# Optimization experiments

Hardware: AMD Instinct MI355X
Metric: run time of the kernel (lower is better)

## Reference

```python
import jax, jax.numpy as jnp
import numpy as np

HID, HEADS, LAYERS, EDIM = 128, 2, 3, 1
HEAD_DIM = HID  # out_channels per head (concat=False -> mean over heads)
N_NODES, N_EDGES = 50000, 500000
LN_EPS = 1e-5


def _layer_norm(x, g, b):
    mu = x.mean(-1, keepdims=True)
    var = ((x - mu) ** 2).mean(-1, keepdims=True)
    return (x - mu) * jax.lax.rsqrt(var + LN_EPS) * g + b


def _transformer_conv(x, src, tgt, edge_attr, Wq, bq, Wk, bk, Wv, bv, We, Wskip, bskip):
    # PyG TransformerConv, concat=False, root_weight=True, lin_edge bias=False
    N = x.shape[0]
    E = src.shape[0]
    q = (x @ Wq + bq).reshape(N, HEADS, HEAD_DIM)
    k = (x @ Wk + bk).reshape(N, HEADS, HEAD_DIM)
    v = (x @ Wv + bv).reshape(N, HEADS, HEAD_DIM)
    e = (edge_attr @ We).reshape(E, HEADS, HEAD_DIM)          # [E,H,C]
    k_j = k[src] + e                                          # gather + edge bias
    q_i = q[tgt]
    alpha = (q_i * k_j).sum(-1) / jnp.sqrt(jnp.asarray(HEAD_DIM, x.dtype))  # [E,H]
    # scatter-softmax over incoming edges of each target node
    m = jax.ops.segment_max(alpha, tgt, num_segments=N)       # [N,H]
    a = jnp.exp(alpha - m[tgt])
    denom = jax.ops.segment_sum(a, tgt, num_segments=N)
    a = a / jnp.where(denom[tgt] > 0, denom[tgt], 1.0)
    msg = (v[src] + e) * a[..., None]                         # [E,H,C]
    out = jax.ops.segment_sum(msg, tgt, num_segments=N)       # [N,H,C]
    out = out.mean(axis=1)                                    # concat=False -> head mean
    return out + x @ Wskip + bskip                            # root/skip connection


def reference(x, edge_index, edge_attr, ln_in_g, ln_in_b,
              Wq, bq, Wk, bk, Wv, bv, We, Wskip, bskip, ln_g, ln_b):
    src, tgt = edge_index[0], edge_index[1]
    x = _layer_norm(x, ln_in_g, ln_in_b)
    for l in range(LAYERS):
        h = _transformer_conv(x, src, tgt, edge_attr,
                              Wq[l], bq[l], Wk[l], bk[l], Wv[l], bv[l],
                              We[l], Wskip[l], bskip[l])
        h = jax.nn.elu(h)
        x = _layer_norm(x + h, ln_g[l], ln_b[l])
    return x


def setup_inputs() -> dict:
    key = jax.random.key(0)
    ks = jax.random.split(key, 12)
    HC = HEADS * HEAD_DIM
    s = 1.0 / np.sqrt(HID)
    inp = {
        "x": jax.random.normal(ks[0], (N_NODES, HID), jnp.float32),
        "edge_index": jax.random.randint(ks[1], (2, N_EDGES), 0, N_NODES, jnp.int64),
        "edge_attr": jax.random.normal(ks[2], (N_EDGES, EDIM), jnp.float32),
        "ln_in_g": jnp.ones((HID,), jnp.float32),
        "ln_in_b": jnp.zeros((HID,), jnp.float32),
        "Wq": jax.random.normal(ks[3], (LAYERS, HID, HC), jnp.float32) * s,
        "bq": jnp.zeros((LAYERS, HC), jnp.float32),
        "Wk": jax.random.normal(ks[4], (LAYERS, HID, HC), jnp.float32) * s,
        "bk": jnp.zeros((LAYERS, HC), jnp.float32),
        "Wv": jax.random.normal(ks[5], (LAYERS, HID, HC), jnp.float32) * s,
        "bv": jnp.zeros((LAYERS, HC), jnp.float32),
        "We": jax.random.normal(ks[6], (LAYERS, EDIM, HC), jnp.float32),
        "Wskip": jax.random.normal(ks[7], (LAYERS, HID, HID), jnp.float32) * s,
        "bskip": jnp.zeros((LAYERS, HID), jnp.float32),
        "ln_g": jnp.ones((LAYERS, HID), jnp.float32),
        "ln_b": jnp.zeros((LAYERS, HID), jnp.float32),
    }
    return inp
```

## Files before the change

kernel.cpp:

```cpp
#include <hip/hip_runtime.h>
#include <math.h>

#define NN 50000
#define NE 500000
#define HIDS 128
#define MCOLS 896
#define NLAYERS 3

typedef __attribute__((ext_vector_type(8))) short short8;
typedef __attribute__((ext_vector_type(4))) float floatx4;
typedef _Float16 half8v __attribute__((ext_vector_type(8)));

#define BSTR 152

static __device__ __forceinline__ unsigned short f2bf(float f) {
    unsigned u = __float_as_uint(f);
    u += 0x7fffu + ((u >> 16) & 1u);
    return (unsigned short)(u >> 16);
}
static __device__ __forceinline__ unsigned short f2h(float f) {
    union { _Float16 h; unsigned short u; } c;
    c.h = (_Float16)f;
    return c.u;
}
#define DPP_ADD(v, ctrl) \
    v += __int_as_float(__builtin_amdgcn_mov_dpp(__float_as_int(v), ctrl, 0xf, 0xf, true))
static __device__ __forceinline__ float wred16(float v) {
    DPP_ADD(v, 0xB1);
    DPP_ADD(v, 0x4E);
    DPP_ADD(v, 0x124);
    DPP_ADD(v, 0x128);
    return v;
}
static __device__ __forceinline__ float wred64(float v) {
    v += __shfl_xor(v, 1, 64);
    v += __shfl_xor(v, 2, 64);
    v += __shfl_xor(v, 4, 64);
    v += __shfl_xor(v, 8, 64);
    v += __shfl_xor(v, 16, 64);
    v += __shfl_xor(v, 32, 64);
    return v;
}

__global__ __launch_bounds__(1024) void eatb_count(const int* __restrict__ tgt, int* __restrict__ cnt) {
    int e = blockIdx.x * 1024 + threadIdx.x;
    if (e < NE) atomicAdd(&cnt[tgt[e]], 1);
}

__global__ __launch_bounds__(256) void eatb_blocksum(const int* __restrict__ cnt, int* __restrict__ bsums) {
    __shared__ int sm[256];
    int i = blockIdx.x * 256 + threadIdx.x;
    sm[threadIdx.x] = (i < NN) ? cnt[i] : 0;
    __syncthreads();
    for (int off = 128; off > 0; off >>= 1) {
        if (threadIdx.x < off) sm[threadIdx.x] += sm[threadIdx.x + off];
        __syncthreads();
    }
    if (threadIdx.x == 0) bsums[blockIdx.x] = sm[0];
}

__global__ __launch_bounds__(256) void eatb_scanb(int* __restrict__ bsums, int nb) {
    __shared__ int sm[256];
    int t = threadIdx.x;
    int v = (t < nb) ? bsums[t] : 0;
    sm[t] = v;
    __syncthreads();
    for (int off = 1; off < 256; off <<= 1) {
        int x = (t >= off) ? sm[t - off] : 0;
        __syncthreads();
        sm[t] += x;
        __syncthreads();
    }
    if (t < nb) bsums[t] = sm[t] - v;
}

__global__ __launch_bounds__(256) void eatb_rowstart(const int* __restrict__ cnt, const int* __restrict__ bsums,
                                                     int* __restrict__ row_start) {
    __shared__ int sm[256];
    int t = threadIdx.x;
    int i = blockIdx.x * 256 + t;
    int v = (i < NN) ? cnt[i] : 0;
    sm[t] = v;
    __syncthreads();
    for (int off = 1; off < 256; off <<= 1) {
        int x = (t >= off) ? sm[t - off] : 0;
        __syncthreads();
        sm[t] += x;
        __syncthreads();
    }
    int excl = sm[t] - v + bsums[blockIdx.x];
    if (i < NN) row_start[i] = excl;
}

__global__ __launch_bounds__(1024) void eatb_scatter(const int* __restrict__ src, const int* __restrict__ tgt,
                                                     const float* __restrict__ ea, int* __restrict__ row_state,
                                                     int2* __restrict__ csr) {
    int e = blockIdx.x * 1024 + threadIdx.x;
    if (e >= NE) return;
    int t = tgt[e];
    int pos = atomicAdd(&row_state[t], 1);
    int2 val;
    val.x = src[e];
    val.y = __float_as_int(ea[e]);
    csr[pos] = val;
}

__global__ __launch_bounds__(256) void eatb_packw(const float* __restrict__ Wq, const float* __restrict__ Wk,
                                                  const float* __restrict__ Wv, const float* __restrict__ Ws,
                                                  const float* __restrict__ bq, const float* __restrict__ bk,
                                                  const float* __restrict__ bv, const float* __restrict__ bs,
                                                  unsigned short* __restrict__ Wt, float* __restrict__ bcat) {
    int idx = blockIdx.x * 256 + threadIdx.x;
    const int WTOT = NLAYERS * MCOLS * HIDS;
    if (idx < WTOT) {
        int l = idx / (MCOLS * HIDS);
        int rem = idx % (MCOLS * HIDS);
        int c = rem / HIDS, k = rem % HIDS;
        float v;
        if (c < 256)      v = Wq[(l * HIDS + k) * 256 + c];
        else if (c < 512) v = Wk[(l * HIDS + k) * 256 + c - 256];
        else if (c < 768) v = Wv[(l * HIDS + k) * 256 + c - 512];
        else              v = Ws[(l * HIDS + k) * 128 + c - 768];
        Wt[idx] = f2bf(v);
    } else {
        int i2 = idx - WTOT;
        if (i2 < NLAYERS * MCOLS) {
            int l = i2 / MCOLS, c = i2 % MCOLS;
            float v;
            if (c < 256)      v = bq[l * 256 + c];
            else if (c < 512) v = bk[l * 256 + c - 256];
            else if (c < 768) v = bv[l * 256 + c - 512];
            else              v = bs[l * 128 + c - 768];
            bcat[i2] = v;
        }
    }
}

__global__ __launch_bounds__(256) void eatb_ln_in(const float* __restrict__ x, const float* __restrict__ g,
                                                  const float* __restrict__ b, float* __restrict__ xout,
                                                  unsigned short* __restrict__ xb) {
    int wid = threadIdx.x >> 6, lane = threadIdx.x & 63;
    int n = blockIdx.x * 4 + wid;
    if (n >= NN) return;
    float2 v = *(const float2*)(x + (size_t)n * HIDS + 2 * lane);
    float mu = wred64(v.x + v.y) * (1.f / 128.f);
    float cx = v.x - mu, cy = v.y - mu;
    float var = wred64(cx * cx + cy * cy) * (1.f / 128.f);
    float r = rsqrtf(var + 1e-5f);
    float2 g2 = *(const float2*)(g + 2 * lane);
    float2 b2 = *(const float2*)(b + 2 * lane);
    float2 o;
    o.x = cx * r * g2.x + b2.x;
    o.y = cy * r * g2.y + b2.y;
    *(float2*)(xout + (size_t)n * HIDS + 2 * lane) = o;
    unsigned pk = (unsigned)f2bf(o.x) | ((unsigned)f2bf(o.y) << 16);
    *(unsigned*)(xb + (size_t)n * HIDS + 2 * lane) = pk;
}

__global__ __launch_bounds__(512, 4) void eatb_gemm(const unsigned short* __restrict__ xb,
                                                    const unsigned short* __restrict__ Wt,
                                                    const float* __restrict__ bias,
                                                    unsigned short* __restrict__ qpack,
                                                    unsigned short* __restrict__ kvpack,
                                                    unsigned short* __restrict__ skipbuf) {
    __shared__ __align__(16) short Bs[64 * BSTR];
    __shared__ __align__(16) float Cs[128 * 68];

    int tid = threadIdx.x;
    int r0 = blockIdx.x * 128;
    int wid = tid >> 6, lane = tid & 63;
    int fr = lane & 15;
    int kq = (lane >> 4) * 8;

    int ar = r0 + wid * 16 + fr;
    bool aok = ar < NN;
    const unsigned short* aptr = xb + (size_t)(aok ? ar : 0) * HIDS;
    short8 afk[4];
    #pragma unroll
    for (int ks = 0; ks < 4; ++ks) afk[ks] = *(const short8*)(aptr + ks * 32 + kq);
    if (!aok) {
        short8 z = {};
        afk[0] = z; afk[1] = z; afk[2] = z; afk[3] = z;
    }

    int brow = tid >> 4, bch = (tid & 15) * 8;
    #pragma unroll
    for (int p = 0; p < 2; ++p) {
        int r = brow + p * 32;
        *(uint4*)(Bs + r * BSTR + bch) = *(const uint4*)(Wt + (size_t)r * HIDS + bch);
    }
    __syncthreads();

    int cl = (tid & 15) * 4;
    for (int ci = 0; ci < 14; ++ci) {
        floatx4 acc[4] = {};
        #pragma unroll
        for (int ks = 0; ks < 4; ++ks) {
            int kof = ks * 32 + kq;
            #pragma unroll
            for (int n = 0; n < 4; ++n) {
                short8 bf = *(const short8*)(Bs + (n * 16 + fr) * BSTR + kof);
                acc[n] = __builtin_amdgcn_mfma_f32_16x16x32_bf16(afk[ks], bf, acc[n], 0, 0, 0);
            }
        }
        #pragma unroll
        for (int n = 0; n < 4; ++n)
            #pragma unroll
            for (int rg = 0; rg < 4; ++rg)
                Cs[(wid * 16 + (lane >> 4) * 4 + rg) * 68 + n * 16 + fr] = acc[n][rg];
        __syncthreads();

        int c0 = ci * 64;
        int C = c0 + cl;
        float4 b4 = *(const float4*)(bias + C);
        #pragma unroll
        for (int p = 0; p < 4; ++p) {
            int rr = (tid >> 4) + 32 * p;
            int gr = r0 + rr;
            if (gr < NN) {
                float4 cv = *(const float4*)(Cs + rr * 68 + cl);
                ushort4 o;
                o.x = f2h(cv.x + b4.x);
                o.y = f2h(cv.y + b4.y);
                o.z = f2h(cv.z + b4.z);
                o.w = f2h(cv.w + b4.w);
                if (C < 256)      *(ushort4*)(qpack + (size_t)gr * 256 + C) = o;
                else if (C < 768) *(ushort4*)(kvpack + (size_t)gr * 512 + (C - 256)) = o;
                else              *(ushort4*)(skipbuf + (size_t)gr * 128 + (C - 768)) = o;
            }
        }
        if (ci < 13) {
            #pragma unroll
            for (int p = 0; p < 2; ++p) {
                int r = brow + p * 32;
                *(uint4*)(Bs + r * BSTR + bch) = *(const uint4*)(Wt + (size_t)((ci + 1) * 64 + r) * HIDS + bch);
            }
        }
        __syncthreads();
    }
}

__global__ __launch_bounds__(256) void eatb_attn(const unsigned short* __restrict__ qpack,
                                                 const unsigned short* __restrict__ kvpack,
                                                 const unsigned short* __restrict__ skipbuf,
                                                 const int2* __restrict__ csr, const int* __restrict__ row_state,
                                                 const float* __restrict__ Wel, const float* __restrict__ g,
                                                 const float* __restrict__ beta, const float* __restrict__ xcur,
                                                 float* __restrict__ dst, unsigned short* __restrict__ xbout) {
    int wid = threadIdx.x >> 6;
    int lane = threadIdx.x & 63;
    int n = blockIdx.x * 4 + wid;
    if (n >= NN) return;
    int slot = lane >> 5;
    int h = (lane >> 4) & 1;
    int sl = lane & 15;
    int dbase = sl * 8;

    const float rs = 0.08838834764831845f;
    const _Float16* qh16 = (const _Float16*)qpack;
    const _Float16* kvh = (const _Float16*)kvpack;

    half8v qh = *(const half8v*)(qh16 + n * 256 + h * 128 + dbase);
    float q0 = (float)qh[0] * rs, q1 = (float)qh[1] * rs, q2 = (float)qh[2] * rs, q3 = (float)qh[3] * rs;
    float q4 = (float)qh[4] * rs, q5 = (float)qh[5] * rs, q6 = (float)qh[6] * rs, q7 = (float)qh[7] * rs;
    const float* wep = Wel + h * 128 + dbase;
    float4 wea = *(const float4*)wep;
    float4 web = *(const float4*)(wep + 4);
    float qwe = wred16(q0 * wea.x + q1 * wea.y + q2 * wea.z + q3 * wea.w +
                       q4 * web.x + q5 * web.y + q6 * web.z + q7 * web.w);

    float sA = 0.f, seaA = 0.f, sB = 0.f, seaB = 0.f;
    float aA0 = 0.f, aA1 = 0.f, aA2 = 0.f, aA3 = 0.f, aA4 = 0.f, aA5 = 0.f, aA6 = 0.f, aA7 = 0.f;
    float aB0 = 0.f, aB1 = 0.f, aB2 = 0.f, aB3 = 0.f, aB4 = 0.f, aB5 = 0.f, aB6 = 0.f, aB7 = 0.f;
    int end = row_state[n];
    int beg = (n > 0) ? row_state[n - 1] : 0;
    int nit = (end - beg + 3) >> 2;
    int lbase = (h << 7) + (sl << 3);
    for (int it = 0; it < nit; ++it) {
        int eA = beg + 4 * it + slot;
        int eB = eA + 2;
        bool vA = eA < end, vB = eB < end;
        int2 seA = csr[vA ? eA : beg];
        int2 seB = csr[vB ? eB : beg];
        int koA = (seA.x << 9) + lbase;
        int koB = (seB.x << 9) + lbase;
        half8v kqA = *(const half8v*)(kvh + koA);
        half8v vqA = *(const half8v*)(kvh + koA + 256);
        half8v kqB = *(const half8v*)(kvh + koB);
        half8v vqB = *(const half8v*)(kvh + koB + 256);
        float eaA = __int_as_float(seA.y);
        float eaB = __int_as_float(seB.y);
        float pA = q0 * (float)kqA[0] + q1 * (float)kqA[1] + q2 * (float)kqA[2] + q3 * (float)kqA[3] +
                   q4 * (float)kqA[4] + q5 * (float)kqA[5] + q6 * (float)kqA[6] + q7 * (float)kqA[7];
        float pB = q0 * (float)kqB[0] + q1 * (float)kqB[1] + q2 * (float)kqB[2] + q3 * (float)kqB[3] +
                   q4 * (float)kqB[4] + q5 * (float)kqB[5] + q6 * (float)kqB[6] + q7 * (float)kqB[7];
        pA = wred16(pA);
        pB = wred16(pB);
        float wA = vA ? __expf(pA + eaA * qwe) : 0.f;
        float wB = vB ? __expf(pB + eaB * qwe) : 0.f;
        sA += wA;
        sB += wB;
        seaA = fmaf(wA, eaA, seaA);
        seaB = fmaf(wB, eaB, seaB);
        aA0 = fmaf(wA, (float)vqA[0], aA0);  aB0 = fmaf(wB, (float)vqB[0], aB0);
        aA1 = fmaf(wA, (float)vqA[1], aA1);  aB1 = fmaf(wB, (float)vqB[1], aB1);
        aA2 = fmaf(wA, (float)vqA[2], aA2);  aB2 = fmaf(wB, (float)vqB[2], aB2);
        aA3 = fmaf(wA, (float)vqA[3], aA3);  aB3 = fmaf(wB, (float)vqB[3], aB3);
        aA4 = fmaf(wA, (float)vqA[4], aA4);  aB4 = fmaf(wB, (float)vqB[4], aB4);
        aA5 = fmaf(wA, (float)vqA[5], aA5);  aB5 = fmaf(wB, (float)vqB[5], aB5);
        aA6 = fmaf(wA, (float)vqA[6], aA6);  aB6 = fmaf(wB, (float)vqB[6], aB6);
        aA7 = fmaf(wA, (float)vqA[7], aA7);  aB7 = fmaf(wB, (float)vqB[7], aB7);
    }
    float s = sA + sB, sea = seaA + seaB;
    float a0 = aA0 + aB0, a1 = aA1 + aB1, a2 = aA2 + aB2, a3 = aA3 + aB3;
    float a4 = aA4 + aB4, a5 = aA5 + aB5, a6 = aA6 + aB6, a7 = aA7 + aB7;

    s += __shfl_xor(s, 32, 64);
    sea += __shfl_xor(sea, 32, 64);
    a0 += __shfl_xor(a0, 32, 64);
    a1 += __shfl_xor(a1, 32, 64);
    a2 += __shfl_xor(a2, 32, 64);
    a3 += __shfl_xor(a3, 32, 64);
    a4 += __shfl_xor(a4, 32, 64);
    a5 += __shfl_xor(a5, 32, 64);
    a6 += __shfl_xor(a6, 32, 64);
    a7 += __shfl_xor(a7, 32, 64);

    float inv = (s > 0.f) ? 1.f / s : 1.f;
    float sw = sea * inv;
    float o0 = a0 * inv + sw * wea.x;
    float o1 = a1 * inv + sw * wea.y;
    float o2 = a2 * inv + sw * wea.z;
    float o3 = a3 * inv + sw * wea.w;
    float o4 = a4 * inv + sw * web.x;
    float o5 = a5 * inv + sw * web.y;
    float o6 = a6 * inv + sw * web.z;
    float o7 = a7 * inv + sw * web.w;
    o0 = 0.5f * (o0 + __shfl_xor(o0, 16, 64));
    o1 = 0.5f * (o1 + __shfl_xor(o1, 16, 64));
    o2 = 0.5f * (o2 + __shfl_xor(o2, 16, 64));
    o3 = 0.5f * (o3 + __shfl_xor(o3, 16, 64));
    o4 = 0.5f * (o4 + __shfl_xor(o4, 16, 64));
    o5 = 0.5f * (o5 + __shfl_xor(o5, 16, 64));
    o6 = 0.5f * (o6 + __shfl_xor(o6, 16, 64));
    o7 = 0.5f * (o7 + __shfl_xor(o7, 16, 64));

    const _Float16* skp = (const _Float16*)skipbuf + n * 128 + dbase;
    half8v skh = *(const half8v*)skp;
    const float* xrp = xcur + n * 128 + dbase;
    float4 xra = *(const float4*)xrp, xrb = *(const float4*)(xrp + 4);
    float y0 = o0 + (float)skh[0], y1 = o1 + (float)skh[1], y2 = o2 + (float)skh[2], y3 = o3 + (float)skh[3];
    float y4 = o4 + (float)skh[4], y5 = o5 + (float)skh[5], y6 = o6 + (float)skh[6], y7 = o7 + (float)skh[7];
    y0 = (y0 > 0.f) ? y0 : __expf(y0) - 1.f;
    y1 = (y1 > 0.f) ? y1 : __expf(y1) - 1.f;
    y2 = (y2 > 0.f) ? y2 : __expf(y2) - 1.f;
    y3 = (y3 > 0.f) ? y3 : __expf(y3) - 1.f;
    y4 = (y4 > 0.f) ? y4 : __expf(y4) - 1.f;
    y5 = (y5 > 0.f) ? y5 : __expf(y5) - 1.f;
    y6 = (y6 > 0.f) ? y6 : __expf(y6) - 1.f;
    y7 = (y7 > 0.f) ? y7 : __expf(y7) - 1.f;
    float p0 = xra.x + y0, p1 = xra.y + y1, p2 = xra.z + y2, p3 = xra.w + y3;
    float p4 = xrb.x + y4, p5 = xrb.y + y5, p6 = xrb.z + y6, p7 = xrb.w + y7;
    float mu = wred16(p0 + p1 + p2 + p3 + p4 + p5 + p6 + p7) * (1.f / 128.f);
    float c0 = p0 - mu, c1 = p1 - mu, c2 = p2 - mu, c3 = p3 - mu;
    float c4 = p4 - mu, c5 = p5 - mu, c6 = p6 - mu, c7 = p7 - mu;
    float var = wred16(c0 * c0 + c1 * c1 + c2 * c2 + c3 * c3 +
                       c4 * c4 + c5 * c5 + c6 * c6 + c7 * c7) * (1.f / 128.f);
    float r = rsqrtf(var + 1e-5f);
    if (lane < 16) {
        const float* gp = g + dbase;
        const float* bp = beta + dbase;
        float4 ga = *(const float4*)gp, gb = *(const float4*)(gp + 4);
        float4 ba = *(const float4*)bp, bb = *(const float4*)(bp + 4);
        float4 oa, ob;
        oa.x = c0 * r * ga.x + ba.x; oa.y = c1 * r * ga.y + ba.y;
        oa.z = c2 * r * ga.z + ba.z; oa.w = c3 * r * ga.w + ba.w;
        ob.x = c4 * r * gb.x + bb.x; ob.y = c5 * r * gb.y + bb.y;
        ob.z = c6 * r * gb.z + bb.z; ob.w = c7 * r * gb.w + bb.w;
        float* dp = dst + n * 128 + dbase;
        *(float4*)dp = oa;
        *(float4*)(dp + 4) = ob;
        if (xbout) {
            uint4 pk;
            pk.x = (unsigned)f2bf(oa.x) | ((unsigned)f2bf(oa.y) << 16);
            pk.y = (unsigned)f2bf(oa.z) | ((unsigned)f2bf(oa.w) << 16);
            pk.z = (unsigned)f2bf(ob.x) | ((unsigned)f2bf(ob.y) << 16);
            pk.w = (unsigned)f2bf(ob.z) | ((unsigned)f2bf(ob.w) << 16);
            *(uint4*)(xbout + n * 128 + dbase) = pk;
        }
    }
}

extern "C" void kernel_launch(void* const* d_in, const int* in_sizes, int n_in,
                              void* d_out, int out_size, void* d_ws, size_t ws_size,
                              hipStream_t stream) {
    const float* x       = (const float*)d_in[0];
    const int*   ei      = (const int*)d_in[1];
    const float* eattr   = (const float*)d_in[2];
    const float* ln_in_g = (const float*)d_in[3];
    const float* ln_in_b = (const float*)d_in[4];
    const float* Wq = (const float*)d_in[5];
    const float* bq = (const float*)d_in[6];
    const float* Wk = (const float*)d_in[7];
    const float* bk = (const float*)d_in[8];
    const float* Wv = (const float*)d_in[9];
    const float* bv = (const float*)d_in[10];
    const float* We = (const float*)d_in[11];
    const float* Ws = (const float*)d_in[12];
    const float* bs = (const float*)d_in[13];
    const float* ln_g = (const float*)d_in[14];
    const float* ln_b = (const float*)d_in[15];
    float* out = (float*)d_out;

    char* p = (char*)d_ws;
    auto carve = [&](size_t bytes) {
        char* r = p;
        p += (bytes + 255) & ~(size_t)255;
        return (void*)r;
    };
    int*  cnt       = (int*)carve((size_t)NN * 4);
    int*  row_state = (int*)carve((size_t)NN * 4);
    int*  bsums     = (int*)carve(1024);
    int2* csr       = (int2*)carve((size_t)NE * 8);
    unsigned short* WcatT = (unsigned short*)carve((size_t)NLAYERS * MCOLS * HIDS * 2);
    float* bcat     = (float*)carve((size_t)NLAYERS * MCOLS * 4);
    float* xcur     = (float*)carve((size_t)NN * HIDS * 4);
    unsigned short* qpack  = (unsigned short*)carve((size_t)NN * 256 * 2);
    unsigned short* kvpack = (unsigned short*)carve((size_t)NN * 512 * 2);
    unsigned short* skipbuf = (unsigned short*)carve((size_t)NN * HIDS * 2);
    unsigned short* xb = (unsigned short*)carve((size_t)NN * HIDS * 2);

    const int NB_N = (NN + 255) / 256;
    const int NB_E1K = (NE + 1023) / 1024;
    const int NODE_BLOCKS = (NN + 3) / 4;

    hipMemsetAsync(cnt, 0, (size_t)NN * 4, stream);
    eatb_count<<<NB_E1K, 1024, 0, stream>>>(ei + NE, cnt);
    eatb_blocksum<<<NB_N, 256, 0, stream>>>(cnt, bsums);
    eatb_scanb<<<1, 256, 0, stream>>>(bsums, NB_N);
    eatb_rowstart<<<NB_N, 256, 0, stream>>>(cnt, bsums, row_state);
    eatb_scatter<<<NB_E1K, 1024, 0, stream>>>(ei, ei + NE, eattr, row_state, csr);

    {
        int tot = NLAYERS * MCOLS * HIDS + NLAYERS * MCOLS;
        eatb_packw<<<(tot + 255) / 256, 256, 0, stream>>>(Wq, Wk, Wv, Ws, bq, bk, bv, bs, WcatT, bcat);
    }

    eatb_ln_in<<<NODE_BLOCKS, 256, 0, stream>>>(x, ln_in_g, ln_in_b, xcur, xb);

    const int GEMM_BLOCKS = (NN + 127) / 128;
    for (int l = 0; l < NLAYERS; ++l) {
        eatb_gemm<<<GEMM_BLOCKS, 512, 0, stream>>>(xb, WcatT + (size_t)l * MCOLS * HIDS,
                                                   bcat + (size_t)l * MCOLS, qpack, kvpack, skipbuf);
        float* dst = (l == NLAYERS - 1) ? out : xcur;
        unsigned short* xbo = (l == NLAYERS - 1) ? nullptr : xb;
        eatb_attn<<<NODE_BLOCKS, 256, 0, stream>>>(qpack, kvpack, skipbuf, csr, row_state,
                                                   We + (size_t)l * 256, ln_g + (size_t)l * 128,
                                                   ln_b + (size_t)l * 128, xcur, dst, xbo);
    }
    (void)in_sizes; (void)n_in; (void)out_size; (void)ws_size;
}
```

Before: 528.9 us.

## Prefetch next edge batch in attention loop, use fdot2 and exp2 with prescaled Q

Software-pipelines the attention edge loop so the CSR entry and the K/V gathers for the next iteration are issued before computing the current one, hiding gather latency. The Q weights and biases are prescaled by 1/sqrt(d)*log2(e) when packed, which lets the per-edge exp become a raw v_exp_f32 and the q·k dot product use packed fp16 fdot2. This costs extra registers for the prefetched buffers, which may lower occupancy, and fdot2 changes the numerics slightly. Because q is scaled before the fp16 store, qwe picks up the log2(e) factor and the exponent stays consistent.

```diff
diff --git a/kernel.cpp b/kernel.cpp
--- a/kernel.cpp
+++ b/kernel.cpp
@@ -10,6 +10,9 @@
 typedef __attribute__((ext_vector_type(8))) short short8;
 typedef __attribute__((ext_vector_type(4))) float floatx4;
 typedef _Float16 half8v __attribute__((ext_vector_type(8)));
+typedef _Float16 half2v __attribute__((ext_vector_type(2)));
+
+union H2U { half8v v; half2v h[4]; };
 
 #define BSTR 152
 
@@ -22,6 +25,11 @@
     union { _Float16 h; unsigned short u; } c;
     c.h = (_Float16)f;
     return c.u;
+}
+static __device__ __forceinline__ float fexp2(float x) {
+    float r;
+    asm("v_exp_f32 %0, %1" : "=v"(r) : "v"(x));
+    return r;
 }
 #define DPP_ADD(v, ctrl) \
     v += __int_as_float(__builtin_amdgcn_mov_dpp(__float_as_int(v), ctrl, 0xf, 0xf, true))
@@ -110,6 +118,7 @@
                                                   const float* __restrict__ bq, const float* __restrict__ bk,
                                                   const float* __restrict__ bv, const float* __restrict__ bs,
                                                   unsigned short* __restrict__ Wt, float* __restrict__ bcat) {
+    const float QS = 0.08838834764831845f * 1.4426950408889634f;
     int idx = blockIdx.x * 256 + threadIdx.x;
     const int WTOT = NLAYERS * MCOLS * HIDS;
     if (idx < WTOT) {
@@ -117,7 +126,7 @@
         int rem = idx % (MCOLS * HIDS);
         int c = rem / HIDS, k = rem % HIDS;
         float v;
-        if (c < 256)      v = Wq[(l * HIDS + k) * 256 + c];
+        if (c < 256)      v = Wq[(l * HIDS + k) * 256 + c] * QS;
         else if (c < 512) v = Wk[(l * HIDS + k) * 256 + c - 256];
         else if (c < 768) v = Wv[(l * HIDS + k) * 256 + c - 512];
         else              v = Ws[(l * HIDS + k) * 128 + c - 768];
@@ -127,7 +136,7 @@
         if (i2 < NLAYERS * MCOLS) {
             int l = i2 / MCOLS, c = i2 % MCOLS;
             float v;
-            if (c < 256)      v = bq[l * 256 + c];
+            if (c < 256)      v = bq[l * 256 + c] * QS;
             else if (c < 512) v = bk[l * 256 + c - 256];
             else if (c < 768) v = bv[l * 256 + c - 512];
             else              v = bs[l * 128 + c - 768];
@@ -256,18 +265,16 @@
     int sl = lane & 15;
     int dbase = sl * 8;
 
-    const float rs = 0.08838834764831845f;
     const _Float16* qh16 = (const _Float16*)qpack;
     const _Float16* kvh = (const _Float16*)kvpack;
 
     half8v qh = *(const half8v*)(qh16 + n * 256 + h * 128 + dbase);
-    float q0 = (float)qh[0] * rs, q1 = (float)qh[1] * rs, q2 = (float)qh[2] * rs, q3 = (float)qh[3] * rs;
-    float q4 = (float)qh[4] * rs, q5 = (float)qh[5] * rs, q6 = (float)qh[6] * rs, q7 = (float)qh[7] * rs;
+    H2U qq; qq.v = qh;
     const float* wep = Wel + h * 128 + dbase;
     float4 wea = *(const float4*)wep;
     float4 web = *(const float4*)(wep + 4);
-    float qwe = wred16(q0 * wea.x + q1 * wea.y + q2 * wea.z + q3 * wea.w +
-                       q4 * web.x + q5 * web.y + q6 * web.z + q7 * web.w);
+    float qwe = wred16((float)qh[0] * wea.x + (float)qh[1] * wea.y + (float)qh[2] * wea.z + (float)qh[3] * wea.w +
+                       (float)qh[4] * web.x + (float)qh[5] * web.y + (float)qh[6] * web.z + (float)qh[7] * web.w);
 
     float sA = 0.f, seaA = 0.f, sB = 0.f, seaB = 0.f;
     float aA0 = 0.f, aA1 = 0.f, aA2 = 0.f, aA3 = 0.f, aA4 = 0.f, aA5 = 0.f, aA6 = 0.f, aA7 = 0.f;
@@ -276,28 +283,53 @@
     int beg = (n > 0) ? row_state[n - 1] : 0;
     int nit = (end - beg + 3) >> 2;
     int lbase = (h << 7) + (sl << 3);
-    for (int it = 0; it < nit; ++it) {
+
+    int2 seA, seB;
+    half8v kqA, vqA, kqB, vqB;
+    bool vA = false, vB = false;
+    int2 nseA, nseB;
+    half8v nkA, nvA, nkB, nvB;
+    bool nvAf = false, nvBf = false;
+
+    auto loadit = [&](int it) {
         int eA = beg + 4 * it + slot;
         int eB = eA + 2;
-        bool vA = eA < end, vB = eB < end;
-        int2 seA = csr[vA ? eA : beg];
-        int2 seB = csr[vB ? eB : beg];
-        int koA = (seA.x << 9) + lbase;
-        int koB = (seB.x << 9) + lbase;
-        half8v kqA = *(const half8v*)(kvh + koA);
-        half8v vqA = *(const half8v*)(kvh + koA + 256);
-        half8v kqB = *(const half8v*)(kvh + koB);
-        half8v vqB = *(const half8v*)(kvh + koB + 256);
+        nvAf = eA < end;
+        nvBf = eB < end;
+        int2 sa = csr[nvAf ? eA : beg];
+        int2 sb = csr[nvBf ? eB : beg];
+        nseA = sa;
+        nseB = sb;
+        int koA = (sa.x << 9) + lbase;
+        int koB = (sb.x << 9) + lbase;
+        nkA = *(const half8v*)(kvh + koA);
+        nvA = *(const half8v*)(kvh + koA + 256);
+        nkB = *(const half8v*)(kvh + koB);
+        nvB = *(const half8v*)(kvh + koB + 256);
+    };
+    auto adopt = [&]() {
+        seA = nseA; seB = nseB;
+        kqA = nkA; vqA = nvA; kqB = nkB; vqB = nvB;
+        vA = nvAf; vB = nvBf;
+    };
+    auto compute = [&]() {
+        H2U ka, kb;
+        ka.v = kqA;
+        kb.v = kqB;
+        float dA0 = __builtin_amdgcn_fdot2(qq.h[0], ka.h[0], 0.f, false);
+        float dA1 = __builtin_amdgcn_fdot2(qq.h[1], ka.h[1], 0.f, false);
+        dA0 = __builtin_amdgcn_fdot2(qq.h[2], ka.h[2], dA0, false);
+        dA1 = __builtin_amdgcn_fdot2(qq.h[3], ka.h[3], dA1, false);
+        float dB0 = __builtin_amdgcn_fdot2(qq.h[0], kb.h[0], 0.f, false);
+        float dB1 = __builtin_amdgcn_fdot2(qq.h[1], kb.h[1], 0.f, false);
+        dB0 = __builtin_amdgcn_fdot2(qq.h[2], kb.h[2], dB0, false);
+        dB1 = __builtin_amdgcn_fdot2(qq.h[3], kb.h[3], dB1, false);
+        float pA = wred16(dA0 + dA1);
+        float pB = wred16(dB0 + dB1);
         float eaA = __int_as_float(seA.y);
         float eaB = __int_as_float(seB.y);
-        float pA = q0 * (float)kqA[0] + q1 * (float)kqA[1] + q2 * (float)kqA[2] + q3 * (float)kqA[3] +
-                   q4 * (float)kqA[4] + q5 * (float)kqA[5] + q6 * (float)kqA[6] + q7 * (float)kqA[7];
-        float pB = q0 * (float)kqB[0] + q1 * (float)kqB[1] + q2 * (float)kqB[2] + q3 * (float)kqB[3] +
-                   q4 * (float)kqB[4] + q5 * (float)kqB[5] + q6 * (float)kqB[6] + q7 * (float)kqB[7];
-        pA = wred16(pA);
-        pB = wred16(pB);
-        float wA = vA ? __expf(pA + eaA * qwe) : 0.f;
-        float wB = vB ? __expf(pB + eaB * qwe) : 0.f;
+        float wA = vA ? fexp2(fmaf(eaA, qwe, pA)) : 0.f;
+        float wB = vB ? fexp2(fmaf(eaB, qwe, pB)) : 0.f;
         sA += wA;
         sB += wB;
         seaA = fmaf(wA, eaA, seaA);
@@ -310,7 +342,19 @@
         aA5 = fmaf(wA, (float)vqA[5], aA5);  aB5 = fmaf(wB, (float)vqB[5], aB5);
         aA6 = fmaf(wA, (float)vqA[6], aA6);  aB6 = fmaf(wB, (float)vqB[6], aB6);
         aA7 = fmaf(wA, (float)vqA[7], aA7);  aB7 = fmaf(wB, (float)vqB[7], aB7);
-    }
+    };
+
+    if (nit > 0) {
+        loadit(0);
+        adopt();
+        for (int it = 1; it < nit; ++it) {
+            loadit(it);
+            compute();
+            adopt();
+        }
+        compute();
+    }
+
     float s = sA + sB, sea = seaA + seaB;
     float a0 = aA0 + aB0, a1 = aA1 + aB1, a2 = aA2 + aB2, a3 = aA3 + aB3;
     float a4 = aA4 + aB4, a5 = aA5 + aB5, a6 = aA6 + aB6, a7 = aA7 + aB7;
```

Result: no change. 527.4 us (-0.3%).
